# Kernel tuning notes

Measured on AMD Instinct MI355X. Metric: run time of the kernel, lower is better.

## Reference

```python
import jax, jax.numpy as jnp
import numpy as np
from functools import partial


def edt_sq(mask):
    """Exact squared Euclidean distance transform (distance from True pixels to
    nearest False pixel), separable two-pass algorithm. mask: bool (..., H, W).
    Matches scipy.ndimage.distance_transform_edt(mask)**2 whenever each 2-D
    slice contains at least one background (False) pixel."""
    H, W = mask.shape[-2], mask.shape[-1]
    LARGE = jnp.float32(H * H + W * W + 1)

    # ---- pass 1: 1-D distance to nearest False along H (rows axis) ----
    mm = jnp.moveaxis(mask, -2, 0)  # (H, ..., W)
    init = jnp.full(mm.shape[1:], LARGE, dtype=jnp.float32)

    def step1(carry, x):
        d = jnp.where(x, carry + 1.0, 0.0)
        return d, d

    _, fwd = jax.lax.scan(step1, init, mm)
    _, bwd = jax.lax.scan(step1, init, mm[::-1])
    d1 = jnp.minimum(fwd, bwd[::-1])            # (H, ..., W) 1-D distance
    f = jnp.minimum(d1 * d1, LARGE)             # squared, capped
    f = jnp.moveaxis(f, 0, -2)                  # (..., H, W)

    # ---- pass 2: D[..., j] = min_k f[..., k] + (j - k)^2 along W ----
    j = jnp.arange(W, dtype=jnp.float32)
    fT = jnp.moveaxis(f, -1, 0)                 # (W, ..., H)

    def step2(D, xk):
        fk, k = xk                               # fk: (..., H)
        cand = fk[..., None] + (j - k) ** 2      # (..., H, W)
        return jnp.minimum(D, cand), None

    D0 = jnp.full(f.shape, LARGE, dtype=jnp.float32)
    D, _ = jax.lax.scan(step2, D0, (fT, j))
    return D


def setup_inputs() -> dict:
    key = jax.random.key(0)
    k1, k2 = jax.random.split(key)
    output = jax.random.normal(k1, (16, 2, 512, 512), dtype=jnp.float32)
    target = jax.random.randint(k2, (16, 512, 512), 0, 2).astype(jnp.int64)
    return {"output": output, "target": target}


def reference(output, target):
    B, C, H, W = output.shape
    probs = jax.nn.softmax(output, axis=1)                    # (B,C,H,W)
    y_onehot = jax.nn.one_hot(target, C, axis=1, dtype=jnp.float32)

    # distance maps only needed for channels 1: (loop starts at c=1)
    pc_mask = probs[:, 1:] > 0.5                              # (B,C-1,H,W)
    gt_mask = y_onehot[:, 1:] > 0.5
    pc_dist_sq = edt_sq(pc_mask)
    gt_dist_sq = edt_sq(gt_mask)
    dist = jax.lax.stop_gradient(pc_dist_sq + gt_dist_sq)     # no_grad in torch

    pred_error = (probs - y_onehot) ** 2                      # (B,C,H,W)
    multipled = pred_error[:, 1:] * dist                      # einsum 'bcxy,bcxy->bcxy'
    return multipled.mean()
```

## Files before the change

### kernel.cpp

```cpp
#include <hip/hip_runtime.h>
#include <hip/hip_fp16.h>

#define BB   16
#define HH   512
#define WW   512
#define HWSZ (HH * WW)
#define NPIX (BB * HWSZ)
#define LARGE_F 524289.0f
#define NW 16
#define GR 8
#define NLOSSBLK (BB * HH / GR)


__global__ __launch_bounds__(512) void pack_kernel(
    const float* __restrict__ out4,
    const int* __restrict__ target,
    unsigned int* __restrict__ bitsG,
    __half* __restrict__ eG) {
  __shared__ unsigned char mbyte[32 * 256];

  const int w    = blockIdx.x >> 1;
  const int half = blockIdx.x & 1;
  const int b    = blockIdx.y;
  const int c0   = half * 256;
  const float* ch0 = out4 + (size_t)(b * 2) * HWSZ;
  const float* ch1 = ch0 + HWSZ;
  const int* tb = target + (size_t)b * HWSZ;
  __half* eb = eG + (size_t)b * HWSZ;

#pragma unroll
  for (int s = 0; s < 4; ++s) {
    int q  = s * 512 + threadIdx.x;
    int i  = q >> 6;
    int cq = (q & 63) * 4;
    int g  = (w * 32 + i) * WW + c0 + cq;
    float4 a0 = *(const float4*)(ch0 + g);
    float4 a1 = *(const float4*)(ch1 + g);
    int4   t4 = *(const int4*)(tb + g);
    unsigned p = 0;
    p |= (unsigned)(((a1.x > a0.x) ? 1u : 0u) | ((t4.x == 1) ? 2u : 0u));
    p |= (unsigned)(((a1.y > a0.y) ? 1u : 0u) | ((t4.y == 1) ? 2u : 0u)) << 8;
    p |= (unsigned)(((a1.z > a0.z) ? 1u : 0u) | ((t4.z == 1) ? 2u : 0u)) << 16;
    p |= (unsigned)(((a1.w > a0.w) ? 1u : 0u) | ((t4.w == 1) ? 2u : 0u)) << 24;
    *(unsigned*)&mbyte[i * 256 + cq] = p;

    float d0, d1, d2, d3;
    d0 = 1.0f / (1.0f + expf(a0.x - a1.x)) - ((t4.x == 1) ? 1.0f : 0.0f);
    d1 = 1.0f / (1.0f + expf(a0.y - a1.y)) - ((t4.y == 1) ? 1.0f : 0.0f);
    d2 = 1.0f / (1.0f + expf(a0.z - a1.z)) - ((t4.z == 1) ? 1.0f : 0.0f);
    d3 = 1.0f / (1.0f + expf(a0.w - a1.w)) - ((t4.w == 1) ? 1.0f : 0.0f);
    __half2 e01 = __floats2half2_rn(d0 * d0, d1 * d1);
    __half2 e23 = __floats2half2_rn(d2 * d2, d3 * d3);
    *(__half2*)(eb + g)     = e01;
    *(__half2*)(eb + g + 2) = e23;
  }
  __syncthreads();

  {
    int c   = threadIdx.x & 255;
    int sel = threadIdx.x >> 8;
    unsigned wd = 0;
#pragma unroll
    for (int k = 0; k < 32; ++k) {
      unsigned mb = mbyte[k * 256 + c];
      wd |= ((mb >> sel) & 1u) << k;
    }
    bitsG[(size_t)((b * 2 + sel) * NW + w) * WW + c0 + c] = wd;
  }
}

__device__ __forceinline__ void colprobe8(const unsigned (*lb)[WW],
                                          const unsigned* __restrict__ gcol,
                                          int wlo, int whi, int j, int i0,
                                          int* __restrict__ rr) {
  const int w = i0 >> 5, bp = i0 & 31;
  const unsigned cur = lb[w - wlo][j];

  unsigned zu = ~cur & (0xFFFFFFFFu >> (31 - bp));
  int up = 0xFFFF;
  if (zu) {
    up = bp - (31 - __clz(zu));
  } else {
    for (int ww = w - 1; ww >= 0; --ww) {
      unsigned z = ~((ww >= wlo) ? lb[ww - wlo][j] : gcol[ww * WW]);
      if (z) { up = i0 - (ww * 32 + 31 - __clz(z)); break; }
    }
  }
  const int bp7 = bp + 7;
  unsigned zd = ~cur & (0xFFFFFFFFu << bp7);
  int dn = 0xFFFF;
  if (zd) {
    dn = (__ffs((int)zd) - 1) - bp7;
  } else {
    for (int ww = w + 1; ww < NW; ++ww) {
      unsigned z = ~((ww <= whi) ? lb[ww - wlo][j] : gcol[ww * WW]);
      if (z) { dn = ww * 32 + (__ffs((int)z) - 1) - (i0 + 7); break; }
    }
  }

  const unsigned bits8 = (cur >> bp) & 0xFFu;
  int ups[GR], dns[GR];
  ups[0] = up;
  for (int k = 1; k < GR; ++k)
    ups[k] = ((bits8 >> k) & 1u) ? ups[k - 1] + 1 : 0;
  dns[GR - 1] = dn;
  for (int k = GR - 2; k >= 0; --k)
    dns[k] = ((bits8 >> k) & 1u) ? dns[k + 1] + 1 : 0;
#pragma unroll
  for (int k = 0; k < GR; ++k) rr[k] = min(ups[k], dns[k]);
}

__global__ __launch_bounds__(512) void loss_kernel(
    const __half* __restrict__ eG,
    const unsigned int* __restrict__ bitsG,
    float* __restrict__ partials) {
  __shared__ unsigned lbits[2][5][WW];
  __shared__ float2 fv[GR][WW];
  __shared__ float ssum[8];

  const int b  = blockIdx.x >> 6;
  const int i0 = (blockIdx.x & 63) * GR;
  const int j  = threadIdx.x;

  const int wc  = i0 >> 5;
  const int wlo = max(0, wc - 2);
  const int whi = min(NW - 1, wc + 2);
  const int nwr = whi - wlo + 1;

  const __half* ep = eG + (size_t)b * HWSZ + (size_t)i0 * WW;
  float ev[GR];
#pragma unroll
  for (int rw = 0; rw < GR; ++rw) ev[rw] = __half2float(ep[rw * WW + j]);

  const unsigned* gb = bitsG + (size_t)(b * 2) * NW * WW;
  const int nquad = nwr * 2 * (WW / 4);
  for (int idx = threadIdx.x; idx < nquad; idx += 512) {
    int cq   = (idx & 127) * 4;
    int rest = idx >> 7;
    int wrel = rest >> 1;
    int sel  = rest & 1;
    uint4 v = *(const uint4*)(gb + (size_t)(sel * NW + wlo + wrel) * WW + cq);
    *(uint4*)&lbits[sel][wrel][cq] = v;
  }
  __syncthreads();

  const unsigned* gpc = gb + j;
  const unsigned* ggt = gb + NW * WW + j;
  int rpc[GR], rgt[GR];
  colprobe8(lbits[0], gpc, wlo, whi, j, i0, rpc);
  colprobe8(lbits[1], ggt, wlo, whi, j, i0, rgt);

  float bpc[GR], bgt[GR];
#pragma unroll
  for (int rw = 0; rw < GR; ++rw) {
    float fpc = (rpc[rw] >= 512) ? LARGE_F : (float)(rpc[rw] * rpc[rw]);
    float fgt = (rgt[rw] >= 512) ? LARGE_F : (float)(rgt[rw] * rgt[rw]);
    fv[rw][j] = make_float2(fpc, fgt);
    bpc[rw] = fpc; bgt[rw] = fgt;
  }
  __syncthreads();

  for (int r = 1; r < WW; ++r) {
    float rr = (float)(r * r);
    float mx = 0.0f;
#pragma unroll
    for (int rw = 0; rw < GR; ++rw) mx = fmaxf(mx, fmaxf(bpc[rw], bgt[rw]));
    if (rr >= mx) break;
    int jl = j - r, jr = j + r;
    if (jl >= 0) {
#pragma unroll
      for (int rw = 0; rw < GR; ++rw) {
        float2 a = fv[rw][jl];
        bpc[rw] = fminf(bpc[rw], a.x + rr);
        bgt[rw] = fminf(bgt[rw], a.y + rr);
      }
    }
    if (jr < WW) {
#pragma unroll
      for (int rw = 0; rw < GR; ++rw) {
        float2 a = fv[rw][jr];
        bpc[rw] = fminf(bpc[rw], a.x + rr);
        bgt[rw] = fminf(bgt[rw], a.y + rr);
      }
    }
  }

  float contrib = 0.0f;
#pragma unroll
  for (int rw = 0; rw < GR; ++rw) contrib += ev[rw] * (bpc[rw] + bgt[rw]);
  contrib *= (1.0f / (float)NPIX);

  for (int off = 32; off > 0; off >>= 1) contrib += __shfl_down(contrib, off);
  int lane = threadIdx.x & 63;
  int wave = threadIdx.x >> 6;
  if (lane == 0) ssum[wave] = contrib;
  __syncthreads();
  if (threadIdx.x == 0) {
    float s = 0.0f;
#pragma unroll
    for (int w = 0; w < 8; ++w) s += ssum[w];
    partials[blockIdx.x] = s;
  }
}

__global__ __launch_bounds__(1024) void reduce_kernel(
    const float* __restrict__ partials, float* __restrict__ d_out) {
  __shared__ float ssum[16];
  float s = partials[threadIdx.x];
  for (int off = 32; off > 0; off >>= 1) s += __shfl_down(s, off);
  int lane = threadIdx.x & 63;
  int wave = threadIdx.x >> 6;
  if (lane == 0) ssum[wave] = s;
  __syncthreads();
  if (threadIdx.x == 0) {
    float t = 0.0f;
#pragma unroll
    for (int w = 0; w < 16; ++w) t += ssum[w];
    *d_out = t;
  }
}

extern "C" void kernel_launch(void* const* d_in, const int* in_sizes, int n_in,
                              void* d_out, int out_size, void* d_ws, size_t ws_size,
                              hipStream_t stream) {
  const float* out4 = (const float*)d_in[0];
  const int* target = (const int*)d_in[1];
  unsigned int* bitsG = (unsigned int*)d_ws;
  __half* eG = (__half*)(bitsG + BB * 2 * NW * WW);
  float* partials = (float*)(eG + NPIX);
  float* out = (float*)d_out;

  dim3 grid1(32, BB);
  pack_kernel<<<grid1, 512, 0, stream>>>(out4, target, bitsG, eG);

  loss_kernel<<<NLOSSBLK, 512, 0, stream>>>(eG, bitsG, partials);

  reduce_kernel<<<1, 1024, 0, stream>>>(partials, out);
}
```

Baseline: 96.51 us.

## Fuse pack, loss and reduce into one cooperative persistent kernel with grid sync

New measurement: 207.1 us. 115% more time.

```diff
diff --git a/kernel.cpp b/kernel.cpp
--- a/kernel.cpp
+++ b/kernel.cpp
@@ -1,5 +1,8 @@
 #include <hip/hip_runtime.h>
 #include <hip/hip_fp16.h>
+#include <hip/hip_cooperative_groups.h>
+
+namespace cg = cooperative_groups;
 
 #define BB   16
 #define HH   512
@@ -9,20 +12,69 @@
 #define LARGE_F 524289.0f
 #define NW 16
 #define GR 8
+#define NBLKC 256
 #define NLOSSBLK (BB * HH / GR)
 
 
-__global__ __launch_bounds__(512) void pack_kernel(
-    const float* __restrict__ out4,
-    const int* __restrict__ target,
-    unsigned int* __restrict__ bitsG,
-    __half* __restrict__ eG) {
-  __shared__ unsigned char mbyte[32 * 256];
-
-  const int w    = blockIdx.x >> 1;
-  const int half = blockIdx.x & 1;
-  const int b    = blockIdx.y;
-  const int c0   = half * 256;
+union SMem {
+  unsigned char mbyte[32 * 256];
+  struct {
+    unsigned lbits[2][5][WW];
+    float2   fv[GR][WW];
+    float    ssum[8];
+  } l;
+};
+
+__device__ __forceinline__ void colprobe8(const unsigned (*lb)[WW],
+                                          const unsigned* __restrict__ gcol,
+                                          int wlo, int whi, int j, int i0,
+                                          int* __restrict__ rr) {
+  const int w = i0 >> 5, bp = i0 & 31;
+  const unsigned cur = lb[w - wlo][j];
+
+  unsigned zu = ~cur & (0xFFFFFFFFu >> (31 - bp));
+  int up = 0xFFFF;
+  if (zu) {
+    up = bp - (31 - __clz(zu));
+  } else {
+    for (int ww = w - 1; ww >= 0; --ww) {
+      unsigned z = ~((ww >= wlo) ? lb[ww - wlo][j] : gcol[ww * WW]);
+      if (z) { up = i0 - (ww * 32 + 31 - __clz(z)); break; }
+    }
+  }
+  const int bp7 = bp + 7;
+  unsigned zd = ~cur & (0xFFFFFFFFu << bp7);
+  int dn = 0xFFFF;
+  if (zd) {
+    dn = (__ffs((int)zd) - 1) - bp7;
+  } else {
+    for (int ww = w + 1; ww < NW; ++ww) {
+      unsigned z = ~((ww <= whi) ? lb[ww - wlo][j] : gcol[ww * WW]);
+      if (z) { dn = ww * 32 + (__ffs((int)z) - 1) - (i0 + 7); break; }
+    }
+  }
+
+  const unsigned bits8 = (cur >> bp) & 0xFFu;
+  int ups[GR], dns[GR];
+  ups[0] = up;
+  for (int k = 1; k < GR; ++k)
+    ups[k] = ((bits8 >> k) & 1u) ? ups[k - 1] + 1 : 0;
+  dns[GR - 1] = dn;
+  for (int k = GR - 2; k >= 0; --k)
+    dns[k] = ((bits8 >> k) & 1u) ? dns[k + 1] + 1 : 0;
+#pragma unroll
+  for (int k = 0; k < GR; ++k) rr[k] = min(ups[k], dns[k]);
+}
+
+__device__ __forceinline__ void pack_unit(
+    int unit, int tid, unsigned char* mbyte,
+    const float* __restrict__ out4, const int* __restrict__ target,
+    unsigned int* __restrict__ bitsG, __half* __restrict__ eG) {
+  const int xb = unit & 31;
+  const int b  = unit >> 5;
+  const int w  = xb >> 1;
+  const int hf = xb & 1;
+  const int c0 = hf * 256;
   const float* ch0 = out4 + (size_t)(b * 2) * HWSZ;
   const float* ch1 = ch0 + HWSZ;
   const int* tb = target + (size_t)b * HWSZ;
@@ -30,7 +82,7 @@
 
 #pragma unroll
   for (int s = 0; s < 4; ++s) {
-    int q  = s * 512 + threadIdx.x;
+    int q  = s * 512 + tid;
     int i  = q >> 6;
     int cq = (q & 63) * 4;
     int g  = (w * 32 + i) * WW + c0 + cq;
@@ -57,8 +109,8 @@
   __syncthreads();
 
   {
-    int c   = threadIdx.x & 255;
-    int sel = threadIdx.x >> 8;
+    int c   = tid & 255;
+    int sel = tid >> 8;
     unsigned wd = 0;
 #pragma unroll
     for (int k = 0; k < 32; ++k) {
@@ -69,58 +121,11 @@
   }
 }
 
-__device__ __forceinline__ void colprobe8(const unsigned (*lb)[WW],
-                                          const unsigned* __restrict__ gcol,
-                                          int wlo, int whi, int j, int i0,
-                                          int* __restrict__ rr) {
-  const int w = i0 >> 5, bp = i0 & 31;
-  const unsigned cur = lb[w - wlo][j];
-
-  unsigned zu = ~cur & (0xFFFFFFFFu >> (31 - bp));
-  int up = 0xFFFF;
-  if (zu) {
-    up = bp - (31 - __clz(zu));
-  } else {
-    for (int ww = w - 1; ww >= 0; --ww) {
-      unsigned z = ~((ww >= wlo) ? lb[ww - wlo][j] : gcol[ww * WW]);
-      if (z) { up = i0 - (ww * 32 + 31 - __clz(z)); break; }
-    }
-  }
-  const int bp7 = bp + 7;
-  unsigned zd = ~cur & (0xFFFFFFFFu << bp7);
-  int dn = 0xFFFF;
-  if (zd) {
-    dn = (__ffs((int)zd) - 1) - bp7;
-  } else {
-    for (int ww = w + 1; ww < NW; ++ww) {
-      unsigned z = ~((ww <= whi) ? lb[ww - wlo][j] : gcol[ww * WW]);
-      if (z) { dn = ww * 32 + (__ffs((int)z) - 1) - (i0 + 7); break; }
-    }
-  }
-
-  const unsigned bits8 = (cur >> bp) & 0xFFu;
-  int ups[GR], dns[GR];
-  ups[0] = up;
-  for (int k = 1; k < GR; ++k)
-    ups[k] = ((bits8 >> k) & 1u) ? ups[k - 1] + 1 : 0;
-  dns[GR - 1] = dn;
-  for (int k = GR - 2; k >= 0; --k)
-    dns[k] = ((bits8 >> k) & 1u) ? dns[k + 1] + 1 : 0;
-#pragma unroll
-  for (int k = 0; k < GR; ++k) rr[k] = min(ups[k], dns[k]);
-}
-
-__global__ __launch_bounds__(512) void loss_kernel(
-    const __half* __restrict__ eG,
-    const unsigned int* __restrict__ bitsG,
-    float* __restrict__ partials) {
-  __shared__ unsigned lbits[2][5][WW];
-  __shared__ float2 fv[GR][WW];
-  __shared__ float ssum[8];
-
-  const int b  = blockIdx.x >> 6;
-  const int i0 = (blockIdx.x & 63) * GR;
-  const int j  = threadIdx.x;
+__device__ __forceinline__ float loss_tile(
+    int tile, int j, SMem& sm,
+    const __half* __restrict__ eG, const unsigned int* __restrict__ bitsG) {
+  const int b  = tile >> 6;
+  const int i0 = (tile & 63) * GR;
 
   const int wc  = i0 >> 5;
   const int wlo = max(0, wc - 2);
@@ -134,28 +139,28 @@
 
   const unsigned* gb = bitsG + (size_t)(b * 2) * NW * WW;
   const int nquad = nwr * 2 * (WW / 4);
-  for (int idx = threadIdx.x; idx < nquad; idx += 512) {
+  for (int idx = j; idx < nquad; idx += 512) {
     int cq   = (idx & 127) * 4;
     int rest = idx >> 7;
     int wrel = rest >> 1;
     int sel  = rest & 1;
     uint4 v = *(const uint4*)(gb + (size_t)(sel * NW + wlo + wrel) * WW + cq);
-    *(uint4*)&lbits[sel][wrel][cq] = v;
+    *(uint4*)&sm.l.lbits[sel][wrel][cq] = v;
   }
   __syncthreads();
 
   const unsigned* gpc = gb + j;
   const unsigned* ggt = gb + NW * WW + j;
   int rpc[GR], rgt[GR];
-  colprobe8(lbits[0], gpc, wlo, whi, j, i0, rpc);
-  colprobe8(lbits[1], ggt, wlo, whi, j, i0, rgt);
+  colprobe8(sm.l.lbits[0], gpc, wlo, whi, j, i0, rpc);
+  colprobe8(sm.l.lbits[1], ggt, wlo, whi, j, i0, rgt);
 
   float bpc[GR], bgt[GR];
 #pragma unroll
   for (int rw = 0; rw < GR; ++rw) {
     float fpc = (rpc[rw] >= 512) ? LARGE_F : (float)(rpc[rw] * rpc[rw]);
     float fgt = (rgt[rw] >= 512) ? LARGE_F : (float)(rgt[rw] * rgt[rw]);
-    fv[rw][j] = make_float2(fpc, fgt);
+    sm.l.fv[rw][j] = make_float2(fpc, fgt);
     bpc[rw] = fpc; bgt[rw] = fgt;
   }
   __syncthreads();
@@ -170,7 +175,7 @@
     if (jl >= 0) {
 #pragma unroll
       for (int rw = 0; rw < GR; ++rw) {
-        float2 a = fv[rw][jl];
+        float2 a = sm.l.fv[rw][jl];
         bpc[rw] = fminf(bpc[rw], a.x + rr);
         bgt[rw] = fminf(bgt[rw], a.y + rr);
       }
@@ -178,27 +183,110 @@
     if (jr < WW) {
 #pragma unroll
       for (int rw = 0; rw < GR; ++rw) {
-        float2 a = fv[rw][jr];
+        float2 a = sm.l.fv[rw][jr];
         bpc[rw] = fminf(bpc[rw], a.x + rr);
         bgt[rw] = fminf(bgt[rw], a.y + rr);
       }
     }
   }
 
+  float c = 0.0f;
+#pragma unroll
+  for (int rw = 0; rw < GR; ++rw) c += ev[rw] * (bpc[rw] + bgt[rw]);
+  return c;
+}
+
+__global__ __launch_bounds__(512) void fused_kernel(
+    const float* __restrict__ out4,
+    const int* __restrict__ target,
+    unsigned int* __restrict__ bitsG,
+    __half* __restrict__ eG,
+    float* __restrict__ partials,
+    unsigned int* __restrict__ counter,
+    float* __restrict__ d_out) {
+  __shared__ SMem sm;
+  __shared__ bool amLast;
+
+  const int tid = threadIdx.x;
+  const int bid = blockIdx.x;
+
+  if (bid == 0 && tid == 0) atomicExch(counter, 0u);
+
+#pragma unroll
+  for (int u = 0; u < 2; ++u) {
+    if (u) __syncthreads();
+    pack_unit(bid + u * NBLKC, tid, sm.mbyte, out4, target, bitsG, eG);
+  }
+
+  __threadfence();
+  cg::this_grid().sync();
+  __threadfence();
+
   float contrib = 0.0f;
-#pragma unroll
-  for (int rw = 0; rw < GR; ++rw) contrib += ev[rw] * (bpc[rw] + bgt[rw]);
+#pragma unroll 1
+  for (int k2 = 0; k2 < 4; ++k2) {
+    __syncthreads();
+    contrib += loss_tile(bid * 4 + k2, tid, sm, eG, bitsG);
+  }
   contrib *= (1.0f / (float)NPIX);
 
+  for (int off = 32; off > 0; off >>= 1) contrib += __shfl_down(contrib, off);
+  const int lane = tid & 63;
+  const int wave = tid >> 6;
+  if (lane == 0) sm.l.ssum[wave] = contrib;
+  __syncthreads();
+  if (tid == 0) {
+    float s = 0.0f;
+#pragma unroll
+    for (int w = 0; w < 8; ++w) s += sm.l.ssum[w];
+    partials[bid] = s;
+    __threadfence();
+    unsigned t = atomicAdd(counter, 1u);
+    amLast = (t == (unsigned)(NBLKC - 1));
+  }
+  __syncthreads();
+
+  if (amLast) {
+    __threadfence();
+    float v = (tid < NBLKC)
+                  ? __hip_atomic_load(&partials[tid], __ATOMIC_RELAXED,
+                                      __HIP_MEMORY_SCOPE_AGENT)
+                  : 0.0f;
+    for (int off = 32; off > 0; off >>= 1) v += __shfl_down(v, off);
+    if (lane == 0) sm.l.ssum[wave] = v;
+    __syncthreads();
+    if (tid == 0) {
+      float s = 0.0f;
+#pragma unroll
+      for (int w = 0; w < 8; ++w) s += sm.l.ssum[w];
+      *d_out = s;
+    }
+  }
+}
+
+__global__ __launch_bounds__(512) void pack_kernel(
+    const float* __restrict__ out4, const int* __restrict__ target,
+    unsigned int* __restrict__ bitsG, __half* __restrict__ eG) {
+  __shared__ unsigned char mbyte[32 * 256];
+  pack_unit(blockIdx.y * 32 + blockIdx.x, threadIdx.x, mbyte, out4, target,
+            bitsG, eG);
+}
+
+__global__ __launch_bounds__(512) void loss_kernel(
+    const __half* __restrict__ eG, const unsigned int* __restrict__ bitsG,
+    float* __restrict__ partials) {
+  __shared__ SMem sm;
+  float contrib = loss_tile(blockIdx.x, threadIdx.x, sm, eG, bitsG);
+  contrib *= (1.0f / (float)NPIX);
   for (int off = 32; off > 0; off >>= 1) contrib += __shfl_down(contrib, off);
   int lane = threadIdx.x & 63;
   int wave = threadIdx.x >> 6;
-  if (lane == 0) ssum[wave] = contrib;
+  if (lane == 0) sm.l.ssum[wave] = contrib;
   __syncthreads();
   if (threadIdx.x == 0) {
     float s = 0.0f;
 #pragma unroll
-    for (int w = 0; w < 8; ++w) s += ssum[w];
+    for (int w = 0; w < 8; ++w) s += sm.l.ssum[w];
     partials[blockIdx.x] = s;
   }
 }
@@ -228,12 +316,36 @@
   unsigned int* bitsG = (unsigned int*)d_ws;
   __half* eG = (__half*)(bitsG + BB * 2 * NW * WW);
   float* partials = (float*)(eG + NPIX);
+  unsigned int* counter = (unsigned int*)(partials + NLOSSBLK);
   float* out = (float*)d_out;
+
+  static int use_coop = -1;
+  if (use_coop < 0) {
+    int coop = 0, nb = 0, ncu = 0;
+    if (hipDeviceGetAttribute(&coop, hipDeviceAttributeCooperativeLaunch, 0) !=
+        hipSuccess)
+      coop = 0;
+    if (hipOccupancyMaxActiveBlocksPerMultiprocessor(&nb, fused_kernel, 512,
+                                                     0) != hipSuccess)
+      nb = 0;
+    if (hipDeviceGetAttribute(&ncu, hipDeviceAttributeMultiprocessorCount, 0) !=
+        hipSuccess)
+      ncu = 0;
+    use_coop = (coop && nb >= 1 && nb * ncu >= NBLKC) ? 1 : 0;
+  }
+
+  if (use_coop) {
+    void* args[] = { (void*)&out4, (void*)&target, (void*)&bitsG, (void*)&eG,
+                     (void*)&partials, (void*)&counter, (void*)&out };
+    hipError_t e = hipLaunchCooperativeKernel(
+        reinterpret_cast<void*>(fused_kernel), dim3(NBLKC), dim3(512), args, 0,
+        stream);
+    if (e == hipSuccess) return;
+    use_coop = 0;
+  }
 
   dim3 grid1(32, BB);
   pack_kernel<<<grid1, 512, 0, stream>>>(out4, target, bitsG, eG);
-
   loss_kernel<<<NLOSSBLK, 512, 0, stream>>>(eG, bitsG, partials);
-
   reduce_kernel<<<1, 1024, 0, stream>>>(partials, out);
 }
```

## Fuse final reduction into loss kernel and shrink shared memory footprint

Applied to the files above, without the earlier changes.

Result: slower. 110.6 us (+14.6%).

```diff
diff --git a/kernel.cpp b/kernel.cpp
--- a/kernel.cpp
+++ b/kernel.cpp
@@ -12,12 +12,67 @@
 #define NLOSSBLK (BB * HH / GR)
 
 
+struct SMemLoss {
+  unsigned lbits[2][3][WW];
+  ushort2  fvs[GR][WW];
+  float    ssum[8];
+};
+
+__device__ __forceinline__ float f_of(unsigned d) {
+  return (d >= 512u) ? LARGE_F : (float)(d * d);
+}
+
+__device__ __forceinline__ void colprobe8(const unsigned (*lb)[WW],
+                                          const unsigned* __restrict__ gcol,
+                                          int wlo, int whi, int j, int i0,
+                                          int* __restrict__ rr) {
+  const int w = i0 >> 5, bp = i0 & 31;
+  const unsigned cur = lb[w - wlo][j];
+
+  unsigned zu = ~cur & (0xFFFFFFFFu >> (31 - bp));
+  int up = 0xFFFF;
+  if (zu) {
+    up = bp - (31 - __clz(zu));
+  } else {
+    for (int ww = w - 1; ww >= 0; --ww) {
+      unsigned z = ~((ww >= wlo) ? lb[ww - wlo][j] : gcol[ww * WW]);
+      if (z) { up = i0 - (ww * 32 + 31 - __clz(z)); break; }
+    }
+  }
+  const int bp7 = bp + 7;
+  unsigned zd = ~cur & (0xFFFFFFFFu << bp7);
+  int dn = 0xFFFF;
+  if (zd) {
+    dn = (__ffs((int)zd) - 1) - bp7;
+  } else {
+    for (int ww = w + 1; ww < NW; ++ww) {
+      unsigned z = ~((ww <= whi) ? lb[ww - wlo][j] : gcol[ww * WW]);
+      if (z) { dn = ww * 32 + (__ffs((int)z) - 1) - (i0 + 7); break; }
+    }
+  }
+
+  const unsigned bits8 = (cur >> bp) & 0xFFu;
+  int ups[GR], dns[GR];
+  ups[0] = up;
+  for (int k = 1; k < GR; ++k)
+    ups[k] = ((bits8 >> k) & 1u) ? ups[k - 1] + 1 : 0;
+  dns[GR - 1] = dn;
+  for (int k = GR - 2; k >= 0; --k)
+    dns[k] = ((bits8 >> k) & 1u) ? dns[k + 1] + 1 : 0;
+#pragma unroll
+  for (int k = 0; k < GR; ++k) rr[k] = min(ups[k], dns[k]);
+}
+
 __global__ __launch_bounds__(512) void pack_kernel(
     const float* __restrict__ out4,
     const int* __restrict__ target,
     unsigned int* __restrict__ bitsG,
-    __half* __restrict__ eG) {
+    __half* __restrict__ eG,
+    unsigned int* __restrict__ counter) {
   __shared__ unsigned char mbyte[32 * 256];
+
+  if (blockIdx.x == 0 && blockIdx.y == 0 && threadIdx.x == 0)
+    atomicExch(counter, 0u);
 
   const int w    = blockIdx.x >> 1;
   const int half = blockIdx.x & 1;
@@ -69,62 +124,22 @@
   }
 }
 
-__device__ __forceinline__ void colprobe8(const unsigned (*lb)[WW],
-                                          const unsigned* __restrict__ gcol,
-                                          int wlo, int whi, int j, int i0,
-                                          int* __restrict__ rr) {
-  const int w = i0 >> 5, bp = i0 & 31;
-  const unsigned cur = lb[w - wlo][j];
-
-  unsigned zu = ~cur & (0xFFFFFFFFu >> (31 - bp));
-  int up = 0xFFFF;
-  if (zu) {
-    up = bp - (31 - __clz(zu));
-  } else {
-    for (int ww = w - 1; ww >= 0; --ww) {
-      unsigned z = ~((ww >= wlo) ? lb[ww - wlo][j] : gcol[ww * WW]);
-      if (z) { up = i0 - (ww * 32 + 31 - __clz(z)); break; }
-    }
-  }
-  const int bp7 = bp + 7;
-  unsigned zd = ~cur & (0xFFFFFFFFu << bp7);
-  int dn = 0xFFFF;
-  if (zd) {
-    dn = (__ffs((int)zd) - 1) - bp7;
-  } else {
-    for (int ww = w + 1; ww < NW; ++ww) {
-      unsigned z = ~((ww <= whi) ? lb[ww - wlo][j] : gcol[ww * WW]);
-      if (z) { dn = ww * 32 + (__ffs((int)z) - 1) - (i0 + 7); break; }
-    }
-  }
-
-  const unsigned bits8 = (cur >> bp) & 0xFFu;
-  int ups[GR], dns[GR];
-  ups[0] = up;
-  for (int k = 1; k < GR; ++k)
-    ups[k] = ((bits8 >> k) & 1u) ? ups[k - 1] + 1 : 0;
-  dns[GR - 1] = dn;
-  for (int k = GR - 2; k >= 0; --k)
-    dns[k] = ((bits8 >> k) & 1u) ? dns[k + 1] + 1 : 0;
-#pragma unroll
-  for (int k = 0; k < GR; ++k) rr[k] = min(ups[k], dns[k]);
-}
-
-__global__ __launch_bounds__(512) void loss_kernel(
+__global__ __launch_bounds__(512, 8) void loss_kernel(
     const __half* __restrict__ eG,
     const unsigned int* __restrict__ bitsG,
-    float* __restrict__ partials) {
-  __shared__ unsigned lbits[2][5][WW];
-  __shared__ float2 fv[GR][WW];
-  __shared__ float ssum[8];
+    float* __restrict__ partials,
+    unsigned int* __restrict__ counter,
+    float* __restrict__ d_out) {
+  __shared__ SMemLoss sm;
+  __shared__ bool amLast;
 
   const int b  = blockIdx.x >> 6;
   const int i0 = (blockIdx.x & 63) * GR;
   const int j  = threadIdx.x;
 
   const int wc  = i0 >> 5;
-  const int wlo = max(0, wc - 2);
-  const int whi = min(NW - 1, wc + 2);
+  const int wlo = max(0, wc - 1);
+  const int whi = min(NW - 1, wc + 1);
   const int nwr = whi - wlo + 1;
 
   const __half* ep = eG + (size_t)b * HWSZ + (size_t)i0 * WW;
@@ -140,23 +155,23 @@
     int wrel = rest >> 1;
     int sel  = rest & 1;
     uint4 v = *(const uint4*)(gb + (size_t)(sel * NW + wlo + wrel) * WW + cq);
-    *(uint4*)&lbits[sel][wrel][cq] = v;
+    *(uint4*)&sm.lbits[sel][wrel][cq] = v;
   }
   __syncthreads();
 
   const unsigned* gpc = gb + j;
   const unsigned* ggt = gb + NW * WW + j;
   int rpc[GR], rgt[GR];
-  colprobe8(lbits[0], gpc, wlo, whi, j, i0, rpc);
-  colprobe8(lbits[1], ggt, wlo, whi, j, i0, rgt);
+  colprobe8(sm.lbits[0], gpc, wlo, whi, j, i0, rpc);
+  colprobe8(sm.lbits[1], ggt, wlo, whi, j, i0, rgt);
 
   float bpc[GR], bgt[GR];
 #pragma unroll
   for (int rw = 0; rw < GR; ++rw) {
-    float fpc = (rpc[rw] >= 512) ? LARGE_F : (float)(rpc[rw] * rpc[rw]);
-    float fgt = (rgt[rw] >= 512) ? LARGE_F : (float)(rgt[rw] * rgt[rw]);
-    fv[rw][j] = make_float2(fpc, fgt);
-    bpc[rw] = fpc; bgt[rw] = fgt;
+    unsigned dpc = (unsigned)min(rpc[rw], 0xFFFF);
+    unsigned dgt = (unsigned)min(rgt[rw], 0xFFFF);
+    sm.fvs[rw][j] = make_ushort2((unsigned short)dpc, (unsigned short)dgt);
+    bpc[rw] = f_of(dpc); bgt[rw] = f_of(dgt);
   }
   __syncthreads();
 
@@ -170,17 +185,17 @@
     if (jl >= 0) {
 #pragma unroll
       for (int rw = 0; rw < GR; ++rw) {
-        float2 a = fv[rw][jl];
-        bpc[rw] = fminf(bpc[rw], a.x + rr);
-        bgt[rw] = fminf(bgt[rw], a.y + rr);
+        ushort2 a = sm.fvs[rw][jl];
+        bpc[rw] = fminf(bpc[rw], f_of(a.x) + rr);
+        bgt[rw] = fminf(bgt[rw], f_of(a.y) + rr);
       }
     }
     if (jr < WW) {
 #pragma unroll
       for (int rw = 0; rw < GR; ++rw) {
-        float2 a = fv[rw][jr];
-        bpc[rw] = fminf(bpc[rw], a.x + rr);
-        bgt[rw] = fminf(bgt[rw], a.y + rr);
+        ushort2 a = sm.fvs[rw][jr];
+        bpc[rw] = fminf(bpc[rw], f_of(a.x) + rr);
+        bgt[rw] = fminf(bgt[rw], f_of(a.y) + rr);
       }
     }
   }
@@ -191,32 +206,36 @@
   contrib *= (1.0f / (float)NPIX);
 
   for (int off = 32; off > 0; off >>= 1) contrib += __shfl_down(contrib, off);
-  int lane = threadIdx.x & 63;
-  int wave = threadIdx.x >> 6;
-  if (lane == 0) ssum[wave] = contrib;
+  const int lane = threadIdx.x & 63;
+  const int wave = threadIdx.x >> 6;
+  if (lane == 0) sm.ssum[wave] = contrib;
   __syncthreads();
   if (threadIdx.x == 0) {
     float s = 0.0f;
 #pragma unroll
-    for (int w = 0; w < 8; ++w) s += ssum[w];
+    for (int w = 0; w < 8; ++w) s += sm.ssum[w];
     partials[blockIdx.x] = s;
-  }
-}
-
-__global__ __launch_bounds__(1024) void reduce_kernel(
-    const float* __restrict__ partials, float* __restrict__ d_out) {
-  __shared__ float ssum[16];
-  float s = partials[threadIdx.x];
-  for (int off = 32; off > 0; off >>= 1) s += __shfl_down(s, off);
-  int lane = threadIdx.x & 63;
-  int wave = threadIdx.x >> 6;
-  if (lane == 0) ssum[wave] = s;
-  __syncthreads();
-  if (threadIdx.x == 0) {
-    float t = 0.0f;
-#pragma unroll
-    for (int w = 0; w < 16; ++w) t += ssum[w];
-    *d_out = t;
+    __threadfence();
+    unsigned t = atomicAdd(counter, 1u);
+    amLast = (t == (unsigned)(NLOSSBLK - 1));
+  }
+  __syncthreads();
+
+  if (amLast) {
+    __threadfence();
+    float v = __hip_atomic_load(&partials[threadIdx.x], __ATOMIC_RELAXED,
+                                __HIP_MEMORY_SCOPE_AGENT) +
+              __hip_atomic_load(&partials[threadIdx.x + 512], __ATOMIC_RELAXED,
+                                __HIP_MEMORY_SCOPE_AGENT);
+    for (int off = 32; off > 0; off >>= 1) v += __shfl_down(v, off);
+    if (lane == 0) sm.ssum[wave] = v;
+    __syncthreads();
+    if (threadIdx.x == 0) {
+      float s = 0.0f;
+#pragma unroll
+      for (int w = 0; w < 8; ++w) s += sm.ssum[w];
+      *d_out = s;
+    }
   }
 }
 
@@ -228,12 +247,11 @@
   unsigned int* bitsG = (unsigned int*)d_ws;
   __half* eG = (__half*)(bitsG + BB * 2 * NW * WW);
   float* partials = (float*)(eG + NPIX);
+  unsigned int* counter = (unsigned int*)(partials + NLOSSBLK);
   float* out = (float*)d_out;
 
   dim3 grid1(32, BB);
-  pack_kernel<<<grid1, 512, 0, stream>>>(out4, target, bitsG, eG);
-
-  loss_kernel<<<NLOSSBLK, 512, 0, stream>>>(eG, bitsG, partials);
-
-  reduce_kernel<<<1, 1024, 0, stream>>>(partials, out);
-}
+  pack_kernel<<<grid1, 512, 0, stream>>>(out4, target, bitsG, eG, counter);
+
+  loss_kernel<<<NLOSSBLK, 512, 0, stream>>>(eG, bitsG, partials, counter, out);
+}
```
